# Kernel tuning notes

Hardware: AMD Instinct MI355X
Metric: run time of the kernel (lower is better)

Reference implementation:

```python
import jax, jax.numpy as jnp
import numpy as np

K = 3            # kernel_size
S = 4            # up_factor
VMAX = 1.0
TAU = 0.5
CENTER_BIAS = 2.5
SMOOTH_RES = 0.15
C_IN = 21
HIDDEN = 48
B_, H0, W0 = 4, 81, 81
CTR = K // 2      # = 1, also GL recursion depth M


def _dir_step_diff(k):
    """Precompute (base_pos - base_neg) per direction/step: [8, M+1, k, k]."""
    c = k // 2
    dirs = np.array([[1, 0], [1, 1], [0, 1], [-1, 1], [-1, 0], [-1, -1], [0, -1], [1, -1]], np.float32)
    dirs = dirs / (np.linalg.norm(dirs, axis=1, keepdims=True) + 1e-8)
    yy, xx = np.meshgrid(np.arange(k), np.arange(k), indexing='ij')
    rel = np.stack([yy - c, xx - c], -1).astype(np.float32)
    diff = np.zeros((8, c + 1, k, k), np.float32)
    for d in range(8):
        v = dirs[d]
        proj = rel[..., 0] * v[1] + rel[..., 1] * v[0]
        step = np.clip(np.round(proj), -c, c).astype(np.int64)
        for m in range(c + 1):
            diff[d, m] = (step == m).astype(np.float32) - (step == -m).astype(np.float32)
    return diff

DIFF = jnp.asarray(_dir_step_diff(K))  # [8, M+1, K, K]


def conv3x3(x, w, b):
    y = jax.lax.conv_general_dilated(x, w, (1, 1), 'SAME',
                                     dimension_numbers=('NCHW', 'OIHW', 'NCHW'))
    return y + b[None, :, None, None]


def bilinear_up(x, s):
    """F.interpolate(scale_factor=s, mode='bilinear', align_corners=True)."""
    B, C, h, w = x.shape
    H, W = h * s, w * s
    ys = jnp.linspace(0.0, h - 1.0, H)
    xs = jnp.linspace(0.0, w - 1.0, W)
    y0 = jnp.clip(jnp.floor(ys).astype(jnp.int32), 0, h - 2)
    x0 = jnp.clip(jnp.floor(xs).astype(jnp.int32), 0, w - 2)
    wy = (ys - y0)[:, None]
    wx = (xs - x0)[None, :]
    x00 = x[:, :, y0][:, :, :, x0]
    x01 = x[:, :, y0][:, :, :, x0 + 1]
    x10 = x[:, :, y0 + 1][:, :, :, x0]
    x11 = x[:, :, y0 + 1][:, :, :, x0 + 1]
    return (x00 * (1 - wy) * (1 - wx) + x01 * (1 - wy) * wx
            + x10 * wy * (1 - wx) + x11 * wy * wx)


def setup_inputs() -> dict:
    key = jax.random.key(0)
    ks = jax.random.split(key, 6)
    wn = lambda k, shape: jax.random.normal(k, shape, jnp.float32) * 0.05
    return {
        'x': jax.random.normal(ks[0], (B_, C_IN, H0, W0), jnp.float32),
        'w1o': wn(ks[1], (HIDDEN, C_IN, 3, 3)), 'b1o': jnp.zeros((HIDDEN,), jnp.float32),
        'w2o': wn(ks[2], (8, HIDDEN, 3, 3)), 'b2o': jnp.zeros((8,), jnp.float32),
        'w1g': wn(ks[3], (HIDDEN, C_IN, 3, 3)), 'b1g': jnp.zeros((HIDDEN,), jnp.float32),
        'w2g': wn(ks[4], (1, HIDDEN, 3, 3)), 'b2g': jnp.zeros((1,), jnp.float32),
        'beta': jnp.asarray(1.6, jnp.float32),
    }


def reference(x, w1o, b1o, w2o, b2o, w1g, b1g, w2g, b2g, beta):
    B, C, h, w = x.shape
    c = CTR
    # heads
    raw_v = conv3x3(jax.nn.relu(conv3x3(x, w1o, b1o)), w2o, b2o)          # [B,8,h,w]
    g = jax.nn.sigmoid(conv3x3(jax.nn.relu(conv3x3(x, w1g, b1g)), w2g, b2g))  # [B,1,h,w]
    v = VMAX * jnp.tanh(raw_v)
    # Gruenwald-Letnikov coefficients, M = center (=1 for k=3)
    coeffs = [jnp.ones_like(v)]
    wm = coeffs[0]
    for m in range(1, c + 1):
        wm = wm * (v - m + 1.0) / m * -1.0
        coeffs.append(wm)
    coeff = jnp.stack(coeffs, axis=2)                                      # [B,8,M+1,h,w]
    # direction kernels, averaged over the 8 directions
    ker = jnp.einsum('bdmhw,dmkl->bklhw', coeff, DIFF) / 8.0               # [B,K,K,h,w]
    mask_pre = ker.reshape(B, K * K, h, w)
    ci = c * K + c
    # NOTE: torch adds center_bias in-place on a view of ker -> ker itself is biased too
    mask_pre = mask_pre.at[:, ci].add(CENTER_BIAS)
    ker_b = mask_pre.reshape(B, K, K, h, w)
    mask_lp = jax.nn.softmax(mask_pre / TAU, axis=1)                       # [B,9,h,w]
    # unfold 3x3 window with reflect padding
    xp = jnp.pad(x, ((0, 0), (0, 0), (c, c), (c, c)), mode='reflect')
    patches = jnp.stack([xp[:, :, i:i + h, j:j + w]
                         for i in range(K) for j in range(K)], axis=2)     # [B,C,9,h,w]
    rep2 = lambda a, ax: jnp.repeat(jnp.repeat(a, S, axis=ax), S, axis=ax + 1)
    neigh = rep2(patches, 3)                                               # [B,C,9,H,W]
    mask_lp_u = rep2(mask_lp, 2)                                           # [B,9,H,W]
    g_up = rep2(g, 2)                                                      # [B,1,H,W]
    x_up = bilinear_up(x, S)                                               # [B,C,H,W]
    y_lp_out = jnp.einsum('bcnHW,bnHW->bcHW', neigh, mask_lp_u)
    lam = SMOOTH_RES * (1.0 - g_up)
    y_lp = x_up + lam * (y_lp_out - x_up)
    # highpass branch (mode='both')
    ker_hp = ker_b - ker_b.mean(axis=(1, 2), keepdims=True)
    ker_hp = ker_hp / (jnp.abs(ker_hp).sum(axis=(1, 2), keepdims=True) + 1e-8)
    mask_hp = rep2(ker_hp.reshape(B, K * K, h, w), 2)
    y_hp = jnp.einsum('bcnHW,bnHW->bcHW', neigh, mask_hp)
    y = y_lp + jnp.tanh(beta) * g_up * y_hp
    return (y, v, g_up)
```

## Files before the change

kernel.cpp:

```cpp
#include <hip/hip_runtime.h>
#include <math.h>

#define B_N   4
#define CIN   21
#define HIDC  48
#define H0    81
#define NP    6561
#define HH    324
#define NPH   104976

__device__ __forceinline__ float tanh_fast(float x) {
    float e = __expf(2.f * x);
    return 1.f - 2.f / (e + 1.f);
}

__global__ __launch_bounds__(256) void k1_conv1(
    const float* __restrict__ x,
    const float* __restrict__ w1o, const float* __restrict__ b1o,
    const float* __restrict__ w1g, const float* __restrict__ b1g,
    float* __restrict__ hid_o, float* __restrict__ hid_g)
{
    __shared__ __align__(16) float wt[189 * 12];
    __shared__ float bs[12];
    const int tid = threadIdx.x;
    const int grp = blockIdx.y;
    const int b   = blockIdx.z;
    const bool head_o = (grp < 4);
    const int ocb = (grp & 3) * 12;
    const float* wsrc = head_o ? w1o : w1g;
    for (int i = tid; i < 189 * 12; i += 256) {
        const int ict = i / 12, oc = i - ict * 12;
        wt[i] = wsrc[(ocb + oc) * 189 + ict];
    }
    if (tid < 12) bs[tid] = (head_o ? b1o : b1g)[ocb + tid];
    __syncthreads();

    const int px = blockIdx.x * 256 + tid;
    const bool valid = (px < NP);
    const int oy = px / H0, ox = px - oy * H0;
    const float* xb = x + (size_t)b * CIN * NP;

    float acc[12];
    #pragma unroll
    for (int j = 0; j < 12; j++) acc[j] = bs[j];

    for (int ic = 0; ic < CIN; ic++) {
        const float* xc = xb + ic * NP;
        float xv[9];
        #pragma unroll
        for (int ky = 0; ky < 3; ky++) {
            const int iy = oy + ky - 1;
            const bool rok = valid && ((unsigned)iy < (unsigned)H0);
            #pragma unroll
            for (int kx = 0; kx < 3; kx++) {
                const int ix = ox + kx - 1;
                const bool ok = rok && ((unsigned)ix < (unsigned)H0);
                xv[ky * 3 + kx] = ok ? xc[iy * H0 + ix] : 0.f;
            }
        }
        #pragma unroll
        for (int tap = 0; tap < 9; tap++) {
            const float4 w0 = *(const float4*)&wt[(ic * 9 + tap) * 12];
            const float4 w1 = *(const float4*)&wt[(ic * 9 + tap) * 12 + 4];
            const float4 w2 = *(const float4*)&wt[(ic * 9 + tap) * 12 + 8];
            const float wj[12] = {w0.x, w0.y, w0.z, w0.w, w1.x, w1.y, w1.z, w1.w,
                                  w2.x, w2.y, w2.z, w2.w};
            const float xvt = xv[tap];
            #pragma unroll
            for (int j = 0; j < 12; j++) acc[j] = fmaf(xvt, wj[j], acc[j]);
        }
    }

    if (valid) {
        float* outp = (head_o ? hid_o : hid_g) + ((size_t)b * HIDC + ocb) * NP + px;
        #pragma unroll
        for (int j = 0; j < 12; j++) outp[j * NP] = fmaxf(acc[j], 0.f);
    }
}

__global__ __launch_bounds__(256) void k2_conv2_masks(
    const float* __restrict__ hid_o, const float* __restrict__ hid_g,
    const float* __restrict__ w2o, const float* __restrict__ b2o,
    const float* __restrict__ w2g, const float* __restrict__ b2g,
    float* __restrict__ v_out,
    float* __restrict__ g_buf, float* __restrict__ m_lp, float* __restrict__ m_hp)
{
    __shared__ __align__(16) float wo_s[HIDC * 9 * 8];
    __shared__ float wg_s[HIDC * 9];
    __shared__ float red[4][32][12];
    __shared__ float res_s[32][28];
    const int tid = threadIdx.x;
    const int b = blockIdx.y;

    for (int i = tid; i < HIDC * 9 * 8; i += 256) {
        const int d = i / (HIDC * 9), r = i - d * (HIDC * 9);
        wo_s[r * 8 + d] = w2o[i];
    }
    for (int i = tid; i < HIDC * 9; i += 256) wg_s[i] = w2g[i];
    __syncthreads();

    const int pxl = tid & 31;
    const int s   = tid >> 5;
    const int w   = tid >> 6;
    const int px  = blockIdx.x * 32 + pxl;
    const bool valid = (px < NP);
    const int oy = px / H0, ox = px - oy * H0;
    const int ic0 = s * 6;
    const float* po = hid_o + ((size_t)b * HIDC + ic0) * NP;
    const float* pg = hid_g + ((size_t)b * HIDC + ic0) * NP;

    float a[8] = {0.f, 0.f, 0.f, 0.f, 0.f, 0.f, 0.f, 0.f};
    float ag = 0.f;

    #pragma unroll 1
    for (int ky = 0; ky < 3; ky++) {
        const int iy = oy + ky - 1;
        const bool rok = valid && ((unsigned)iy < (unsigned)H0);
        #pragma unroll
        for (int kx = 0; kx < 3; kx++) {
            const int ix = ox + kx - 1;
            const bool ok = rok && ((unsigned)ix < (unsigned)H0);
            const int off = iy * H0 + ix;
            const int tap = ky * 3 + kx;
            #pragma unroll
            for (int j = 0; j < 6; j++) {
                const float vo = ok ? po[j * NP + off] : 0.f;
                const float vg = ok ? pg[j * NP + off] : 0.f;
                const int wb = ((ic0 + j) * 9 + tap) * 8;
                const float4 wA = *(const float4*)&wo_s[wb];
                const float4 wB = *(const float4*)&wo_s[wb + 4];
                a[0] = fmaf(vo, wA.x, a[0]); a[1] = fmaf(vo, wA.y, a[1]);
                a[2] = fmaf(vo, wA.z, a[2]); a[3] = fmaf(vo, wA.w, a[3]);
                a[4] = fmaf(vo, wB.x, a[4]); a[5] = fmaf(vo, wB.y, a[5]);
                a[6] = fmaf(vo, wB.z, a[6]); a[7] = fmaf(vo, wB.w, a[7]);
                ag = fmaf(vg, wg_s[(ic0 + j) * 9 + tap], ag);
            }
        }
    }

    #pragma unroll
    for (int n = 0; n < 8; n++) a[n] += __shfl_xor(a[n], 32);
    ag += __shfl_xor(ag, 32);
    if ((tid & 32) == 0) {
        #pragma unroll
        for (int n = 0; n < 8; n++) red[w][pxl][n] = a[n];
        red[w][pxl][8] = ag;
    }
    __syncthreads();

    if (tid < 32 && valid) {
        float v[8];
        #pragma unroll
        for (int n = 0; n < 8; n++)
            v[n] = tanh_fast(red[0][tid][n] + red[1][tid][n] + red[2][tid][n]
                             + red[3][tid][n] + b2o[n]);
        const float agf = red[0][tid][8] + red[1][tid][8] + red[2][tid][8]
                        + red[3][tid][8] + b2g[0];
        const float g = 1.f / (1.f + __expf(-agf));

        constexpr float DT[8][9] = {
            {-1, 0, 1, -1, 0, 1, -1, 0, 1},
            {-1,-1, 0, -1, 0, 1,  0, 1, 1},
            {-1,-1,-1,  0, 0, 0,  1, 1, 1},
            { 0,-1,-1,  1, 0,-1,  1, 1, 0},
            { 1, 0,-1,  1, 0,-1,  1, 0,-1},
            { 1, 1, 0,  1, 0,-1,  0,-1,-1},
            { 1, 1, 1,  0, 0, 0, -1,-1,-1},
            { 0, 1, 1, -1, 0, 1, -1,-1, 0}};
        float ker[9];
        #pragma unroll
        for (int n = 0; n < 9; n++) {
            float t = 0.f;
            #pragma unroll
            for (int d = 0; d < 8; d++) t += v[d] * DT[d][n];
            ker[n] = -0.125f * t;
        }
        ker[4] += 2.5f;
        float mx = ker[0];
        #pragma unroll
        for (int n = 1; n < 9; n++) mx = fmaxf(mx, ker[n]);
        float exn[9], sum = 0.f;
        #pragma unroll
        for (int n = 0; n < 9; n++) { exn[n] = __expf((ker[n] - mx) * 2.0f); sum += exn[n]; }
        const float rs = 1.f / sum;
        float mean = 0.f;
        #pragma unroll
        for (int n = 0; n < 9; n++) mean += ker[n];
        mean *= (1.f / 9.f);
        float den = 1e-8f;
        #pragma unroll
        for (int n = 0; n < 9; n++) den += fabsf(ker[n] - mean);
        const float rd = 1.f / den;

        #pragma unroll
        for (int n = 0; n < 8; n++) res_s[tid][n] = v[n];
        res_s[tid][8] = g;
        #pragma unroll
        for (int n = 0; n < 9; n++) {
            res_s[tid][9 + n]  = exn[n] * rs;
            res_s[tid][18 + n] = (ker[n] - mean) * rd;
        }
    }
    __syncthreads();

    const int px0 = blockIdx.x * 32;
    for (int j = tid; j < 27 * 32; j += 256) {
        const int plane = j >> 5, pl = j & 31;
        const int p = px0 + pl;
        if (p >= NP) continue;
        const float val = res_s[pl][plane];
        float* dst;
        if (plane < 8)        dst = v_out + ((size_t)b * 8 + plane) * NP;
        else if (plane == 8)  dst = g_buf + (size_t)b * NP;
        else if (plane < 18)  dst = m_lp + ((size_t)b * 9 + (plane - 9)) * NP;
        else                  dst = m_hp + ((size_t)b * 9 + (plane - 18)) * NP;
        dst[p] = val;
    }
}

__global__ __launch_bounds__(256) void k4_up(
    const float* __restrict__ x, const float* __restrict__ g_buf,
    const float* __restrict__ m_lp, const float* __restrict__ m_hp,
    const float* __restrict__ beta,
    float* __restrict__ y_out, float* __restrict__ gup_out)
{
    __shared__ float ml_s[9][81];
    __shared__ float mh_s[9][81];
    __shared__ float g_s[81];
    __shared__ float xrow[3][11][84];
    __shared__ float alp_s[11][84];
    __shared__ float ahp_s[11][84];
    const int tid  = threadIdx.x;
    const int h0r  = blockIdx.x;
    const int ygrp = blockIdx.y;
    const int b    = blockIdx.z;
    const int c0   = ygrp * 11;
    const int nc   = (ygrp == 0) ? 11 : 10;

    const int rb = h0r * H0;
    for (int i = tid; i < 19 * 81; i += 256) {
        const int pl = i / 81, wq = i - pl * 81;
        if (pl < 9)       ml_s[pl][wq] = m_lp[((size_t)b * 9 + pl) * NP + rb + wq];
        else if (pl < 18) mh_s[pl - 9][wq] = m_hp[((size_t)b * 9 + (pl - 9)) * NP + rb + wq];
        else              g_s[wq] = g_buf[(size_t)b * NP + rb + wq];
    }
    const int r0 = (h0r == 0) ? 1 : h0r - 1;
    const int r2 = (h0r == H0 - 1) ? H0 - 2 : h0r + 1;
    const int rr[3] = {r0, h0r, r2};
    for (int i = tid; i < 3 * nc * 81; i += 256) {
        const int t = i / (nc * 81), rem = i - t * nc * 81;
        const int cc = rem / 81, wq = rem - cc * 81;
        xrow[t][cc][wq] = x[((size_t)b * CIN + c0 + cc) * NP + rr[t] * H0 + wq];
    }
    __syncthreads();

    for (int i = tid; i < nc * 81; i += 256) {
        const int cc = i / 81, wq = i - cc * 81;
        const int xm = (wq == 0) ? 1 : wq - 1;
        const int xp = (wq == H0 - 1) ? H0 - 2 : wq + 1;
        float alp = 0.f, ahp = 0.f;
        #pragma unroll
        for (int t = 0; t < 3; t++) {
            const float p0 = xrow[t][cc][xm];
            const float p1 = xrow[t][cc][wq];
            const float p2 = xrow[t][cc][xp];
            alp += p0 * ml_s[t * 3 + 0][wq] + p1 * ml_s[t * 3 + 1][wq] + p2 * ml_s[t * 3 + 2][wq];
            ahp += p0 * mh_s[t * 3 + 0][wq] + p1 * mh_s[t * 3 + 1][wq] + p2 * mh_s[t * 3 + 2][wq];
        }
        alp_s[cc][wq] = alp;
        ahp_s[cc][wq] = ahp;
    }
    __syncthreads();

    const float tb = tanh_fast(beta[0]);
    for (int i = tid; i < 11 * 4 * 81; i += 256) {
        const int pl = i / 324, rem = i - pl * 324;
        const int dh = rem / 81, wq = rem - dh * 81;
        const int H = h0r * 4 + dh;
        if (ygrp == 1 && pl == 10) {
            const float g = g_s[wq];
            *reinterpret_cast<float4*>(gup_out + (size_t)b * NPH + H * HH + wq * 4) =
                make_float4(g, g, g, g);
            continue;
        }
        const int cc = pl;
        const int c = c0 + pl;
        const float g = g_s[wq];
        const float lam = 0.15f * (1.f - g);
        const float gh = tb * g;
        const float alp = alp_s[cc][wq];
        const float ahp = ahp_s[cc][wq];
        const float ysf = (float)H * (80.f / 323.f);
        int y0 = (int)ysf;
        if (y0 > H0 - 2) y0 = H0 - 2;
        const float wy = ysf - (float)y0;
        const int sy = y0 - h0r + 1;
        const int xm = (wq == 0) ? 1 : wq - 1;
        const int xp = (wq == H0 - 1) ? H0 - 2 : wq + 1;
        const float a0 = xrow[sy][cc][(wq == 0) ? 0 : xm];
        const float a1 = xrow[sy][cc][wq];
        const float a2 = xrow[sy][cc][(wq == H0 - 1) ? H0 - 1 : xp];
        const float b0 = xrow[sy + 1][cc][(wq == 0) ? 0 : xm];
        const float b1 = xrow[sy + 1][cc][wq];
        const float b2 = xrow[sy + 1][cc][(wq == H0 - 1) ? H0 - 1 : xp];
        float res[4];
        #pragma unroll
        for (int k = 0; k < 4; k++) {
            const int W = wq * 4 + k;
            const float xsf = (float)W * (80.f / 323.f);
            int x0 = (int)xsf;
            if (x0 > H0 - 2) x0 = H0 - 2;
            const float wx = xsf - (float)x0;
            const int sx = x0 - wq + 1;
            const float top = (sx == 0) ? a0 + (a1 - a0) * wx : a1 + (a2 - a1) * wx;
            const float bot = (sx == 0) ? b0 + (b1 - b0) * wx : b1 + (b2 - b1) * wx;
            const float xup = top + (bot - top) * wy;
            res[k] = xup + lam * (alp - xup) + gh * ahp;
        }
        *reinterpret_cast<float4*>(y_out + ((size_t)b * CIN + c) * NPH + H * HH + wq * 4) =
            make_float4(res[0], res[1], res[2], res[3]);
    }
}

extern "C" void kernel_launch(void* const* d_in, const int* in_sizes, int n_in,
                              void* d_out, int out_size, void* d_ws, size_t ws_size,
                              hipStream_t stream)
{
    const float* x    = (const float*)d_in[0];
    const float* w1o  = (const float*)d_in[1];
    const float* b1o  = (const float*)d_in[2];
    const float* w2o  = (const float*)d_in[3];
    const float* b2o  = (const float*)d_in[4];
    const float* w1g  = (const float*)d_in[5];
    const float* b1g  = (const float*)d_in[6];
    const float* w2g  = (const float*)d_in[7];
    const float* b2g  = (const float*)d_in[8];
    const float* beta = (const float*)d_in[9];
    float* out = (float*)d_out;
    float* wsf = (float*)d_ws;

    float* hid_o = wsf;
    float* hid_g = hid_o + (size_t)B_N * HIDC * NP;
    float* m_lp  = hid_g + (size_t)B_N * HIDC * NP;
    float* m_hp  = m_lp + (size_t)B_N * 9 * NP;
    float* g_buf = m_hp + (size_t)B_N * 9 * NP;

    float* y_out = out;
    float* v_out = out + (size_t)B_N * CIN * NPH;
    float* gup   = v_out + (size_t)B_N * 8 * NP;

    k1_conv1<<<dim3((NP + 255) / 256, 8, B_N), 256, 0, stream>>>(
        x, w1o, b1o, w1g, b1g, hid_o, hid_g);
    k2_conv2_masks<<<dim3((NP + 31) / 32, B_N), 256, 0, stream>>>(
        hid_o, hid_g, w2o, b2o, w2g, b2g, v_out, g_buf, m_lp, m_hp);
    k4_up<<<dim3(H0, 2, B_N), 256, 0, stream>>>(x, g_buf, m_lp, m_hp, beta, y_out, gup);
}
```

Baseline: 153.3 us.

## Read conv weights directly via scalar loads instead of staging in LDS

Both conv kernels stop copying weights into shared memory and instead index the global weight arrays directly. The weight addresses are uniform across each block, so the compiler can use scalar (SGPR) loads and skip the LDS staging loop and its barrier. k1 also precomputes the nine tap offsets and boundary masks once per thread. k2 moves to 512-thread blocks covering 64 pixels with eight channel slices, which drops the cross-wave shuffle reduction and fully unrolls the tap loop. The cost is relying on scalar-cache hits for the weights and using more registers.

```diff
diff --git a/kernel.cpp b/kernel.cpp
--- a/kernel.cpp
+++ b/kernel.cpp
@@ -20,54 +20,45 @@
     const float* __restrict__ w1g, const float* __restrict__ b1g,
     float* __restrict__ hid_o, float* __restrict__ hid_g)
 {
-    __shared__ __align__(16) float wt[189 * 12];
-    __shared__ float bs[12];
     const int tid = threadIdx.x;
     const int grp = blockIdx.y;
     const int b   = blockIdx.z;
     const bool head_o = (grp < 4);
     const int ocb = (grp & 3) * 12;
-    const float* wsrc = head_o ? w1o : w1g;
-    for (int i = tid; i < 189 * 12; i += 256) {
-        const int ict = i / 12, oc = i - ict * 12;
-        wt[i] = wsrc[(ocb + oc) * 189 + ict];
-    }
-    if (tid < 12) bs[tid] = (head_o ? b1o : b1g)[ocb + tid];
-    __syncthreads();
+    const float* __restrict__ wsrc = head_o ? w1o : w1g;
+    const float* __restrict__ bsrc = head_o ? b1o : b1g;
 
     const int px = blockIdx.x * 256 + tid;
     const bool valid = (px < NP);
     const int oy = px / H0, ox = px - oy * H0;
     const float* xb = x + (size_t)b * CIN * NP;
 
+    int off[9];
+    float msk[9];
+    #pragma unroll
+    for (int t = 0; t < 9; t++) {
+        const int dy = t / 3 - 1, dx = t % 3 - 1;
+        const int iy = oy + dy, ix = ox + dx;
+        const bool ok = valid && ((unsigned)iy < (unsigned)H0) && ((unsigned)ix < (unsigned)H0);
+        off[t] = ok ? iy * H0 + ix : 0;
+        msk[t] = ok ? 1.f : 0.f;
+    }
+
     float acc[12];
     #pragma unroll
-    for (int j = 0; j < 12; j++) acc[j] = bs[j];
+    for (int j = 0; j < 12; j++) acc[j] = bsrc[ocb + j];
 
     for (int ic = 0; ic < CIN; ic++) {
         const float* xc = xb + ic * NP;
         float xv[9];
         #pragma unroll
-        for (int ky = 0; ky < 3; ky++) {
-            const int iy = oy + ky - 1;
-            const bool rok = valid && ((unsigned)iy < (unsigned)H0);
+        for (int t = 0; t < 9; t++) xv[t] = xc[off[t]] * msk[t];
+        #pragma unroll
+        for (int tap = 0; tap < 9; tap++) {
+            const int wi = ic * 9 + tap;
             #pragma unroll
-            for (int kx = 0; kx < 3; kx++) {
-                const int ix = ox + kx - 1;
-                const bool ok = rok && ((unsigned)ix < (unsigned)H0);
-                xv[ky * 3 + kx] = ok ? xc[iy * H0 + ix] : 0.f;
-            }
-        }
-        #pragma unroll
-        for (int tap = 0; tap < 9; tap++) {
-            const float4 w0 = *(const float4*)&wt[(ic * 9 + tap) * 12];
-            const float4 w1 = *(const float4*)&wt[(ic * 9 + tap) * 12 + 4];
-            const float4 w2 = *(const float4*)&wt[(ic * 9 + tap) * 12 + 8];
-            const float wj[12] = {w0.x, w0.y, w0.z, w0.w, w1.x, w1.y, w1.z, w1.w,
-                                  w2.x, w2.y, w2.z, w2.w};
-            const float xvt = xv[tap];
-            #pragma unroll
-            for (int j = 0; j < 12; j++) acc[j] = fmaf(xvt, wj[j], acc[j]);
+            for (int j = 0; j < 12; j++)
+                acc[j] = fmaf(xv[tap], wsrc[(ocb + j) * 189 + wi], acc[j]);
         }
     }
 
@@ -78,31 +69,21 @@
     }
 }
 
-__global__ __launch_bounds__(256) void k2_conv2_masks(
+__global__ __launch_bounds__(512) void k2_conv2_masks(
     const float* __restrict__ hid_o, const float* __restrict__ hid_g,
     const float* __restrict__ w2o, const float* __restrict__ b2o,
     const float* __restrict__ w2g, const float* __restrict__ b2g,
     float* __restrict__ v_out,
     float* __restrict__ g_buf, float* __restrict__ m_lp, float* __restrict__ m_hp)
 {
-    __shared__ __align__(16) float wo_s[HIDC * 9 * 8];
-    __shared__ float wg_s[HIDC * 9];
-    __shared__ float red[4][32][12];
-    __shared__ float res_s[32][28];
-    const int tid = threadIdx.x;
-    const int b = blockIdx.y;
-
-    for (int i = tid; i < HIDC * 9 * 8; i += 256) {
-        const int d = i / (HIDC * 9), r = i - d * (HIDC * 9);
-        wo_s[r * 8 + d] = w2o[i];
-    }
-    for (int i = tid; i < HIDC * 9; i += 256) wg_s[i] = w2g[i];
-    __syncthreads();
-
-    const int pxl = tid & 31;
-    const int s   = tid >> 5;
-    const int w   = tid >> 6;
-    const int px  = blockIdx.x * 32 + pxl;
+    __shared__ float red[8][64][10];
+    __shared__ float res_s[64][28];
+    const int tid  = threadIdx.x;
+    const int lane = tid & 63;
+    const int s    = tid >> 6;
+    const int b    = blockIdx.y;
+    const int px0  = blockIdx.x * 64;
+    const int px   = px0 + lane;
     const bool valid = (px < NP);
     const int oy = px / H0, ox = px - oy * H0;
     const int ic0 = s * 6;
@@ -112,7 +93,7 @@
     float a[8] = {0.f, 0.f, 0.f, 0.f, 0.f, 0.f, 0.f, 0.f};
     float ag = 0.f;
 
-    #pragma unroll 1
+    #pragma unroll
     for (int ky = 0; ky < 3; ky++) {
         const int iy = oy + ky - 1;
         const bool rok = valid && ((unsigned)iy < (unsigned)H0);
@@ -120,42 +101,38 @@
         for (int kx = 0; kx < 3; kx++) {
             const int ix = ox + kx - 1;
             const bool ok = rok && ((unsigned)ix < (unsigned)H0);
-            const int off = iy * H0 + ix;
+            const int offp = iy * H0 + ix;
             const int tap = ky * 3 + kx;
             #pragma unroll
             for (int j = 0; j < 6; j++) {
-                const float vo = ok ? po[j * NP + off] : 0.f;
-                const float vg = ok ? pg[j * NP + off] : 0.f;
-                const int wb = ((ic0 + j) * 9 + tap) * 8;
-                const float4 wA = *(const float4*)&wo_s[wb];
-                const float4 wB = *(const float4*)&wo_s[wb + 4];
-                a[0] = fmaf(vo, wA.x, a[0]); a[1] = fmaf(vo, wA.y, a[1]);
-                a[2] = fmaf(vo, wA.z, a[2]); a[3] = fmaf(vo, wA.w, a[3]);
-                a[4] = fmaf(vo, wB.x, a[4]); a[5] = fmaf(vo, wB.y, a[5]);
-                a[6] = fmaf(vo, wB.z, a[6]); a[7] = fmaf(vo, wB.w, a[7]);
-                ag = fmaf(vg, wg_s[(ic0 + j) * 9 + tap], ag);
+                const float vo = ok ? po[j * NP + offp] : 0.f;
+                const float vg = ok ? pg[j * NP + offp] : 0.f;
+                const int wi = (ic0 + j) * 9 + tap;
+                #pragma unroll
+                for (int d = 0; d < 8; d++)
+                    a[d] = fmaf(vo, w2o[d * (HIDC * 9) + wi], a[d]);
+                ag = fmaf(vg, w2g[wi], ag);
             }
         }
     }
 
     #pragma unroll
-    for (int n = 0; n < 8; n++) a[n] += __shfl_xor(a[n], 32);
-    ag += __shfl_xor(ag, 32);
-    if ((tid & 32) == 0) {
-        #pragma unroll
-        for (int n = 0; n < 8; n++) red[w][pxl][n] = a[n];
-        red[w][pxl][8] = ag;
-    }
+    for (int n = 0; n < 8; n++) red[s][lane][n] = a[n];
+    red[s][lane][8] = ag;
     __syncthreads();
 
-    if (tid < 32 && valid) {
+    if (tid < 64 && valid) {
         float v[8];
         #pragma unroll
-        for (int n = 0; n < 8; n++)
-            v[n] = tanh_fast(red[0][tid][n] + red[1][tid][n] + red[2][tid][n]
-                             + red[3][tid][n] + b2o[n]);
-        const float agf = red[0][tid][8] + red[1][tid][8] + red[2][tid][8]
-                        + red[3][tid][8] + b2g[0];
+        for (int n = 0; n < 8; n++) {
+            float t = 0.f;
+            #pragma unroll
+            for (int w = 0; w < 8; w++) t += red[w][tid][n];
+            v[n] = tanh_fast(t + b2o[n]);
+        }
+        float agf = b2g[0];
+        #pragma unroll
+        for (int w = 0; w < 8; w++) agf += red[w][tid][8];
         const float g = 1.f / (1.f + __expf(-agf));
 
         constexpr float DT[8][9] = {
@@ -203,9 +180,8 @@
     }
     __syncthreads();
 
-    const int px0 = blockIdx.x * 32;
-    for (int j = tid; j < 27 * 32; j += 256) {
-        const int plane = j >> 5, pl = j & 31;
+    for (int j = tid; j < 27 * 64; j += 512) {
+        const int plane = j >> 6, pl = j & 63;
         const int p = px0 + pl;
         if (p >= NP) continue;
         const float val = res_s[pl][plane];
@@ -351,7 +327,7 @@
 
     k1_conv1<<<dim3((NP + 255) / 256, 8, B_N), 256, 0, stream>>>(
         x, w1o, b1o, w1g, b1g, hid_o, hid_g);
-    k2_conv2_masks<<<dim3((NP + 31) / 32, B_N), 256, 0, stream>>>(
+    k2_conv2_masks<<<dim3((NP + 63) / 64, B_N), 512, 0, stream>>>(
         hid_o, hid_g, w2o, b2o, w2g, b2g, v_out, g_buf, m_lp, m_hp);
     k4_up<<<dim3(H0, 2, B_N), 256, 0, stream>>>(x, g_buf, m_lp, m_hp, beta, y_out, gup);
 }
```

After: 345.7 us. 125% more time.
